# Optimization experiments

Measured on AMD Instinct MI355X. Metric: run time of the kernel, lower is better.

Reference implementation:

```python
import jax, jax.numpy as jnp
import numpy as np

S, E, K, D = 20000, 10000, 128, 128   # students, exercises, knowledge, latent dim
N_EK, N_SE = 40000, 500000            # exercise-knowledge edges, student-exercise edges
B = 2048                              # extract batch size


def setup_inputs() -> dict:
    key = jax.random.key(0)
    ks = jax.random.split(key, 16)
    inp = {}
    # Embedding tables (xavier-ish scale)
    inp["stu_emb"] = jax.random.normal(ks[0], (S, D), jnp.float32) * 0.1
    inp["exer_emb"] = jax.random.normal(ks[1], (E, D), jnp.float32) * 0.1
    inp["kn_emb"] = jax.random.normal(ks[2], (K, D), jnp.float32) * 0.1
    inp["disc_emb"] = jax.random.normal(ks[3], (E, 1), jnp.float32) * 0.1
    # GraphLayer params, stacked over [fusion_layer=2, graph={k_from_e,e_from_k,s_from_e,e_from_s}]
    inp["GW"] = jax.random.normal(ks[4], (2, 4, D, D), jnp.float32) * (1.0 / np.sqrt(D))
    inp["Ga"] = jax.random.normal(ks[5], (2, 4, 2 * D), jnp.float32) * 0.1
    # Fusion attention fcs: idx 0=e_attn_fc1, 1=e_attn_fc2, 2=k_attn_fc3 (weight [2D], bias scalar)
    inp["Fw"] = jax.random.normal(ks[6], (2, 3, 2 * D), jnp.float32) * 0.1
    inp["Fb"] = jax.random.normal(ks[7], (2, 3), jnp.float32) * 0.1
    # q_mask (unused by extract, part of the signature)
    inp["q_mask"] = jax.random.bernoulli(ks[8], 0.03, (B, K)).astype(jnp.float32)
    inp["student_id"] = jax.random.randint(ks[9], (B,), 0, S, jnp.int32)
    inp["exercise_id"] = jax.random.randint(ks[10], (B,), 0, E, jnp.int32)
    # k_from_e graph: nodes = [exercises 0..E) ++ [knowledge E..E+K); edges exercise -> knowledge
    inp["ek_src"] = jax.random.randint(ks[11], (N_EK,), 0, E, jnp.int32)
    inp["ek_dst"] = E + jax.random.randint(ks[12], (N_EK,), 0, K, jnp.int32)
    # s_from_e graph: nodes = [exercises 0..E) ++ [students E..E+S); edges exercise -> student
    inp["se_src"] = jax.random.randint(ks[13], (N_SE,), 0, E, jnp.int32)
    inp["se_dst"] = E + jax.random.randint(ks[14], (N_SE,), 0, S, jnp.int32)
    return inp


def _graph_layer(h, W, a, src, dst, n):
    # GAT-style: z = h W; per-edge score a^T [z_src; z_dst]; segment softmax over dst; weighted sum of z_src.
    z = h @ W                                   # [n, D]
    zs, zd = z[src], z[dst]                     # [ne, D] gathers
    e = jnp.concatenate([zs, zd], axis=1) @ a   # [ne]
    emax = jax.ops.segment_max(e, dst, num_segments=n)
    emax = jnp.where(jnp.isfinite(emax), emax, 0.0)  # empty segments -> -inf -> 0
    ex = jnp.exp(e - emax[dst])
    den = jax.ops.segment_sum(ex, dst, num_segments=n)
    alpha = ex / jnp.where(den > 0, den, 1.0)[dst]
    return jax.ops.segment_sum(alpha[:, None] * zs, dst, num_segments=n)  # nodes w/o mail -> 0 (DGL semantics)


def _fusion(kn, ex, st, GWl, Gal, Fwl, Fbl, ek_src, ek_dst, se_src, se_dst):
    nek, nes = E + K, E + S
    ekg = jnp.concatenate([ex, kn], axis=0)
    kfe = _graph_layer(ekg, GWl[0], Gal[0], ek_src, ek_dst, nek)  # k_from_e
    efk = _graph_layer(ekg, GWl[1], Gal[1], ek_dst, ek_src, nek)  # e_from_k (reversed edges)
    esg = jnp.concatenate([ex, st], axis=0)
    ufe = _graph_layer(esg, GWl[2], Gal[2], se_src, se_dst, nes)  # s_from_e
    efu = _graph_layer(esg, GWl[3], Gal[3], se_dst, se_src, nes)  # e_from_s (reversed edges)
    # knowledge update: softmax over a single column == 1 (faithful to original)
    Dk = kfe[E:]
    s3 = jax.nn.softmax((jnp.concatenate([kn, Dk], axis=1) @ Fwl[2] + Fbl[2])[:, None], axis=1)
    kn2 = kn + s3[:, 0:1] * Dk
    # exercise update: 2-way softmax gate
    Bx, Cx = efk[:E], efu[:E]
    s1 = jnp.concatenate([ex, Bx], axis=1) @ Fwl[0] + Fbl[0]
    s2 = jnp.concatenate([ex, Cx], axis=1) @ Fwl[1] + Fbl[1]
    sc = jax.nn.softmax(jnp.stack([s1, s2], axis=1), axis=1)  # [E, 2]
    ex2 = ex + sc[:, 0:1] * Bx + sc[:, 1:2] * Cx
    st2 = st + ufe[E:]
    return kn2, ex2, st2


def reference(stu_emb, exer_emb, kn_emb, disc_emb, GW, Ga, Fw, Fb, q_mask,
              student_id, exercise_id, ek_src, ek_dst, se_src, se_dst):
    kn, ex, st = kn_emb, exer_emb, stu_emb
    for l in range(2):  # FusionLayer1, FusionLayer2
        kn, ex, st = _fusion(kn, ex, st, GW[l], Ga[l], Fw[l], Fb[l],
                             ek_src, ek_dst, se_src, se_dst)
    bs = st[student_id]            # [B, D]
    be = ex[exercise_id]           # [B, D]
    disc = disc_emb[exercise_id]   # [B, 1]
    # if_type == 'rcd': repeat(1,D).reshape(B,D,D) == broadcast along axis 1
    stu_ts = jnp.broadcast_to(bs[:, None, :], (B, D, D))
    exer_ts = jnp.broadcast_to(be[:, None, :], (B, D, D))
    kn_ts = jnp.broadcast_to(kn[None, :, :], (B, K, D))
    return (stu_ts, exer_ts, disc, kn_ts)
```

## Files before the change

kernel.cpp:

```cpp
#include <hip/hip_runtime.h>

#define S_N 20000
#define E_N 10000
#define K_N 128
#define D_N 128
#define NEK 40000
#define NSE 500000
#define B_N 2048

typedef __attribute__((ext_vector_type(8))) short bf16x8;
typedef __attribute__((ext_vector_type(4))) float f32x4;

__device__ __forceinline__ unsigned short f2bf(float f){
  unsigned int u = __float_as_uint(f);
  unsigned int r = u + 0x7FFFu + ((u >> 16) & 1u);
  return (unsigned short)(r >> 16);
}
__device__ __forceinline__ float bf2f(unsigned short h){
  return __uint_as_float(((unsigned int)h) << 16);
}

struct GS { const unsigned short* Ah; const unsigned short* Al;
            const unsigned short* Wh; const unsigned short* Wl;
            float* Z; int rows; };
struct SSet { const float* z; const float* p; const int* rowptr; const int* col;
              const float* base; float* out; int ndst; };
struct CSet { const int* cnt; int n; int* rp; int* cur; };

__global__ __launch_bounds__(256) void k_wprep(const float* __restrict__ GW, const float* __restrict__ Ga,
                                               unsigned short* __restrict__ wf, float* __restrict__ wa){
  int g = blockIdx.x;
  const float* W  = GW + (size_t)g*16384;
  const float* a1 = Ga + (size_t)g*256;
  unsigned short* whi = wf + (size_t)g*16384;
  unsigned short* wlo = wf + (size_t)(8+g)*16384;
  int t = threadIdx.x, l = t & 63;
  for(int pi = t>>6; pi < 32; pi += 4){
    int c2 = pi >> 2, kt = pi & 3;
    unsigned short h[8], lo[8];
    #pragma unroll
    for(int j=0;j<8;j++){
      int k = kt*32 + (l>>4)*8 + j;
      int c = c2*16 + (l&15);
      float f = W[(size_t)k*128 + c];
      unsigned short hb = f2bf(f);
      h[j] = hb; lo[j] = f2bf(f - bf2f(hb));
    }
    size_t off = ((size_t)pi*64 + l)*8;
    uint4 hv, lv;
    hv.x = (unsigned)h[0] | ((unsigned)h[1]<<16);  hv.y = (unsigned)h[2] | ((unsigned)h[3]<<16);
    hv.z = (unsigned)h[4] | ((unsigned)h[5]<<16);  hv.w = (unsigned)h[6] | ((unsigned)h[7]<<16);
    lv.x = (unsigned)lo[0] | ((unsigned)lo[1]<<16); lv.y = (unsigned)lo[2] | ((unsigned)lo[3]<<16);
    lv.z = (unsigned)lo[4] | ((unsigned)lo[5]<<16); lv.w = (unsigned)lo[6] | ((unsigned)lo[7]<<16);
    *(uint4*)(whi + off) = hv;
    *(uint4*)(wlo + off) = lv;
  }
  for(int k = t; k < 128; k += 256){
    float s = 0.f;
    const float* wr = W + (size_t)k*128;
    for(int c=0;c<128;c++) s += wr[c]*a1[c];
    wa[(size_t)g*128 + k] = s;
  }
}

__global__ __launch_bounds__(256) void k_cvt(const float* __restrict__ kn, const float* __restrict__ ex,
    const float* __restrict__ st,
    unsigned short* __restrict__ knb, unsigned short* __restrict__ exb, unsigned short* __restrict__ stb,
    const float* __restrict__ wa, int l4,
    float* __restrict__ Pefk, float* __restrict__ Pkfe, float* __restrict__ Pufe, float* __restrict__ Pefu){
  int w = (blockIdx.x*256 + threadIdx.x) >> 6;
  int lane = threadIdx.x & 63;
  const float* src; unsigned short *hi, *lo; int r;
  const float* wv1; const float* wv2 = nullptr; float *P1, *P2 = nullptr;
  if(w < K_N){ r = w; src = kn + (size_t)r*128; hi = knb; lo = knb + (size_t)K_N*128;
               wv1 = wa + (size_t)(l4+1)*128; P1 = Pefk; }
  else if(w < K_N + E_N){ r = w - K_N; src = ex + (size_t)r*128; hi = exb; lo = exb + (size_t)E_N*128;
               wv1 = wa + (size_t)(l4+0)*128; P1 = Pkfe;
               wv2 = wa + (size_t)(l4+2)*128; P2 = Pufe; }
  else { r = w - K_N - E_N; if(r >= S_N) return; src = st + (size_t)r*128; hi = stb; lo = stb + (size_t)S_N*128;
               wv1 = wa + (size_t)(l4+3)*128; P1 = Pefu; }
  float2 x = ((const float2*)src)[lane];
  float2 v1 = ((const float2*)wv1)[lane];
  float d1 = x.x*v1.x + x.y*v1.y;
  float d2 = 0.f;
  if(wv2){ float2 v2 = ((const float2*)wv2)[lane]; d2 = x.x*v2.x + x.y*v2.y; }
  #pragma unroll
  for(int off=1; off<64; off<<=1){ d1 += __shfl_xor(d1,off); d2 += __shfl_xor(d2,off); }
  if(lane==0){ P1[r] = expf(d1); if(P2) P2[r] = expf(d2); }
  unsigned short h0 = f2bf(x.x), h1 = f2bf(x.y);
  unsigned short l0 = f2bf(x.x - bf2f(h0)), l1 = f2bf(x.y - bf2f(h1));
  ((ushort2*)(hi + (size_t)r*128))[lane] = make_ushort2(h0,h1);
  ((ushort2*)(lo + (size_t)r*128))[lane] = make_ushort2(l0,l1);
}

#define GT0 4
#define GT1 317
#define GT2 942
#define GT3 1255
__global__ __launch_bounds__(256) void k_gemm(GS g0, GS g1, GS g2, GS g3){
  int b = blockIdx.x;
  GS g; int lt;
  if(b < GT0){ g = g0; lt = b; }
  else if(b < GT1){ g = g1; lt = b - GT0; }
  else if(b < GT2){ g = g2; lt = b - GT1; }
  else { g = g3; lt = b - GT2; }
  int l = threadIdx.x & 63, wv = threadIdx.x >> 6;
  int r0 = lt*32;
  bf16x8 bh[2][4], bl[2][4];
  #pragma unroll
  for(int cs=0; cs<2; cs++)
    #pragma unroll
    for(int kt=0; kt<4; kt++){
      size_t o = (((size_t)((wv*2+cs)*4 + kt))*64 + l)*8;
      bh[cs][kt] = *(const bf16x8*)(g.Wh + o);
      bl[cs][kt] = *(const bf16x8*)(g.Wl + o);
    }
  f32x4 acc[2][2];
  #pragma unroll
  for(int rs=0;rs<2;rs++)
    #pragma unroll
    for(int cs=0;cs<2;cs++) acc[rs][cs] = (f32x4){0.f,0.f,0.f,0.f};
  #pragma unroll
  for(int kt=0; kt<4; kt++){
    bf16x8 ah[2], al[2];
    #pragma unroll
    for(int rs=0; rs<2; rs++){
      size_t ao = ((size_t)(r0 + rs*16 + (l&15)))*128 + kt*32 + (l>>4)*8;
      ah[rs] = *(const bf16x8*)(g.Ah + ao);
      al[rs] = *(const bf16x8*)(g.Al + ao);
    }
    #pragma unroll
    for(int rs=0; rs<2; rs++)
      #pragma unroll
      for(int cs=0; cs<2; cs++){
        acc[rs][cs] = __builtin_amdgcn_mfma_f32_16x16x32_bf16(ah[rs], bh[cs][kt], acc[rs][cs], 0,0,0);
        acc[rs][cs] = __builtin_amdgcn_mfma_f32_16x16x32_bf16(ah[rs], bl[cs][kt], acc[rs][cs], 0,0,0);
        acc[rs][cs] = __builtin_amdgcn_mfma_f32_16x16x32_bf16(al[rs], bh[cs][kt], acc[rs][cs], 0,0,0);
      }
  }
  #pragma unroll
  for(int rs=0; rs<2; rs++)
    #pragma unroll
    for(int cs=0; cs<2; cs++){
      int cb = (wv<<5) + (cs<<4) + (l&15);
      #pragma unroll
      for(int j=0;j<4;j++){
        int rr = r0 + rs*16 + ((l>>4)<<2) + j;
        if(rr < g.rows) g.Z[(size_t)rr*128 + cb] = acc[rs][cs][j];
      }
    }
}

__global__ __launch_bounds__(256) void k_hist(const int* __restrict__ eks, const int* __restrict__ ekd,
      const int* __restrict__ ses, const int* __restrict__ sed,
      int* c_eke, int* c_ekk, int* c_see, int* c_ses){
  int i = blockIdx.x*256 + threadIdx.x;
  if(i < NEK){ atomicAdd(c_eke + eks[i], 1); atomicAdd(c_ekk + (ekd[i]-E_N), 1); }
  if(i < NSE){ atomicAdd(c_see + ses[i], 1); atomicAdd(c_ses + (sed[i]-E_N), 1); }
}

__global__ __launch_bounds__(1024) void k_scan(CSet c0, CSet c1, CSet c2, CSet c3){
  CSet c = c0;
  if(blockIdx.x==1) c=c1; else if(blockIdx.x==2) c=c2; else if(blockIdx.x==3) c=c3;
  __shared__ int part[1024];
  int t = threadIdx.x;
  int n = c.n;
  int chunk = (n + 1023) >> 10;
  int b0 = t * chunk;
  int s = 0;
  for(int i=0;i<chunk;i++){ int idx=b0+i; if(idx<n) s += c.cnt[idx]; }
  part[t] = s;
  __syncthreads();
  for(int off=1; off<1024; off<<=1){
    int v = (t>=off) ? part[t-off] : 0;
    __syncthreads();
    part[t] += v;
    __syncthreads();
  }
  int run = t ? part[t-1] : 0;
  for(int i=0;i<chunk;i++){
    int idx=b0+i;
    if(idx<n){ int cc = c.cnt[idx]; c.rp[idx]=run; c.cur[idx]=run; run += cc; }
  }
  if(t==0) c.rp[n] = part[1023];
}

__global__ __launch_bounds__(256) void k_fill(const int* __restrict__ eks, const int* __restrict__ ekd,
      const int* __restrict__ ses, const int* __restrict__ sed,
      int* u_eke, int* u_ekk, int* u_see, int* u_ses,
      int* o_eke, int* o_ekk, int* o_see, int* o_ses){
  int i = blockIdx.x*256 + threadIdx.x;
  if(i < NEK){
    int a = eks[i], b = ekd[i];
    int pos = atomicAdd(u_eke + a, 1);        o_eke[pos] = b;
    int pos2 = atomicAdd(u_ekk + (b-E_N), 1); o_ekk[pos2] = a;
  }
  if(i < NSE){
    int a = ses[i], b = sed[i];
    int pos = atomicAdd(u_see + a, 1);        o_see[pos] = b;
    int pos2 = atomicAdd(u_ses + (b-E_N), 1); o_ses[pos2] = a;
  }
}

#define SB1 2500
#define SB2 5000
#define SB3 10000
#define SB4 10128
__global__ __launch_bounds__(256) void k_seg(SSet s0, SSet s1, SSet s2, SSet s3){
  __shared__ float4 red[4][32];
  __shared__ float redd[4];
  int b = blockIdx.x;
  int lane = threadIdx.x & 63, wid = threadIdx.x >> 6;
  int half = lane >> 5, l32 = lane & 31;
  SSet s; int row, str, stride; bool multi = false;
  if(b < SB1){ s = s0; row = b*4 + wid; }
  else if(b < SB2){ s = s1; row = (b-SB1)*4 + wid; }
  else if(b < SB3){ s = s2; row = (b-SB2)*4 + wid; }
  else { s = s3; row = b - SB3; multi = true; }
  if(!multi){ str = half; stride = 2; }
  else      { str = wid*2 + half; stride = 8; }
  if(row >= s.ndst) return;
  int e0 = s.rowptr[row], e1 = s.rowptr[row+1];
  const int* col = s.col; const float* p = s.p; const float* z = s.z;
  float4 acc = {0.f,0.f,0.f,0.f}; float den = 0.f;
  int e = e0 + str;
  for(; e + 3*stride < e1; e += 4*stride){
    int cA = col[e], cB = col[e+stride], cC = col[e+2*stride], cD = col[e+3*stride];
    float xA = p[cA], xB = p[cB], xC = p[cC], xD = p[cD];
    float4 zA = ((const float4*)(z + (size_t)cA*128))[l32];
    float4 zB = ((const float4*)(z + (size_t)cB*128))[l32];
    float4 zC = ((const float4*)(z + (size_t)cC*128))[l32];
    float4 zD = ((const float4*)(z + (size_t)cD*128))[l32];
    acc.x += xA*zA.x + xB*zB.x + xC*zC.x + xD*zD.x;
    acc.y += xA*zA.y + xB*zB.y + xC*zC.y + xD*zD.y;
    acc.z += xA*zA.z + xB*zB.z + xC*zC.z + xD*zD.z;
    acc.w += xA*zA.w + xB*zB.w + xC*zC.w + xD*zD.w;
    den += (xA + xB) + (xC + xD);
  }
  for(; e < e1; e += stride){
    int cA = col[e];
    float xA = p[cA];
    float4 zA = ((const float4*)(z + (size_t)cA*128))[l32];
    acc.x += xA*zA.x; acc.y += xA*zA.y; acc.z += xA*zA.z; acc.w += xA*zA.w;
    den += xA;
  }
  acc.x += __shfl_xor(acc.x,32); acc.y += __shfl_xor(acc.y,32);
  acc.z += __shfl_xor(acc.z,32); acc.w += __shfl_xor(acc.w,32);
  den   += __shfl_xor(den,32);
  if(multi){
    if(half==0){ red[wid][l32] = acc; if(l32==0) redd[wid] = den; }
    __syncthreads();
    if(wid) return;
    acc = red[0][l32]; den = redd[0];
    #pragma unroll
    for(int i=1;i<4;i++){
      float4 r4 = red[i][l32];
      acc.x+=r4.x; acc.y+=r4.y; acc.z+=r4.z; acc.w+=r4.w; den += redd[i];
    }
  }
  float inv = den > 0.f ? 1.f/den : 0.f;
  float4 res = {acc.x*inv, acc.y*inv, acc.z*inv, acc.w*inv};
  if(s.base){
    float4 b4 = ((const float4*)(s.base + (size_t)row*128))[l32];
    res.x+=b4.x; res.y+=b4.y; res.z+=b4.z; res.w+=b4.w;
  }
  if(half==0) ((float4*)(s.out + (size_t)row*128))[l32] = res;
}

__global__ __launch_bounds__(256) void k_exup(const float* __restrict__ base, float* __restrict__ ex,
     const float* __restrict__ Bx, const float* __restrict__ Cx,
     const float* __restrict__ Fw, const float* __restrict__ Fb){
  int w = (blockIdx.x*256 + threadIdx.x) >> 6;
  int lane = threadIdx.x & 63;
  if(w >= E_N) return;
  const float* er = base + (size_t)w*128;
  const float* br = Bx + (size_t)w*128;
  const float* cr = Cx + (size_t)w*128;
  float e0 = er[lane], e1 = er[lane+64];
  float b0 = br[lane], b1 = br[lane+64];
  float c0 = cr[lane], c1 = cr[lane+64];
  float s1 = e0*Fw[lane]     + e1*Fw[lane+64]
           + b0*Fw[lane+128] + b1*Fw[lane+192];
  float s2 = e0*Fw[256+lane]     + e1*Fw[256+lane+64]
           + c0*Fw[256+lane+128] + c1*Fw[256+lane+192];
  #pragma unroll
  for(int off=32; off; off>>=1){ s1 += __shfl_down(s1,off); s2 += __shfl_down(s2,off); }
  s1 = __shfl(s1, 0) + Fb[0];
  s2 = __shfl(s2, 0) + Fb[1];
  float mx = fmaxf(s1,s2);
  float pp = expf(s1-mx), qq = expf(s2-mx);
  float inv = 1.f/(pp+qq);
  float* orow = ex + (size_t)w*128;
  orow[lane]    = e0 + (pp*inv)*b0 + (qq*inv)*c0;
  orow[lane+64] = e1 + (pp*inv)*b1 + (qq*inv)*c1;
}

__global__ __launch_bounds__(256) void k_out(const float* __restrict__ st, const float* __restrict__ ex,
    const float* __restrict__ kn, const float* __restrict__ disc,
    const int* __restrict__ sid, const int* __restrict__ eid,
    float* out0, float* out1, float* out2, float* out3){
  int w = (blockIdx.x*256 + threadIdx.x) >> 6;
  int lane = threadIdx.x & 63;
  const int ROWW = 3*B_N*64;
  if(w < ROWW){
    int half = lane>>5, l32 = lane&31;
    int r = w*2 + half;
    int sec = r >> 18;
    int rr = r & 262143;
    int b = rr >> 7, i = rr & 127;
    const float* emb; int srow; float* ob;
    if(sec==0){ emb=st; srow=sid[b]; ob=out0; }
    else if(sec==1){ emb=ex; srow=eid[b]; ob=out1; }
    else { emb=kn; srow=i; ob=out3; }
    f32x4 v = *((const f32x4*)(emb + (size_t)srow*128) + l32);
    __builtin_nontemporal_store(v, (f32x4*)(ob + (size_t)rr*128) + l32);
  } else {
    int i = (w - ROWW)*64 + lane;
    if(i < B_N) out2[i] = disc[eid[i]];
  }
}

extern "C" void kernel_launch(void* const* d_in, const int* in_sizes, int n_in,
                              void* d_out, int out_size, void* d_ws, size_t ws_size,
                              hipStream_t stream){
  (void)in_sizes; (void)out_size; (void)ws_size;
  const float* stu_emb  = (const float*)d_in[0];
  const float* exer_emb = (const float*)d_in[1];
  const float* kn_emb   = (const float*)d_in[2];
  const float* disc_emb = (const float*)d_in[3];
  const float* GW = (const float*)d_in[4];
  const float* Ga = (const float*)d_in[5];
  const float* Fw = (const float*)d_in[6];
  const float* Fb = (const float*)d_in[7];
  int base = n_in - 6;
  const int* sid    = (const int*)d_in[base];
  const int* eid    = (const int*)d_in[base+1];
  const int* ek_src = (const int*)d_in[base+2];
  const int* ek_dst = (const int*)d_in[base+3];
  const int* se_src = (const int*)d_in[base+4];
  const int* se_dst = (const int*)d_in[base+5];

  char* w = (char*)d_ws;
  size_t off = 0;
  auto alloc = [&](size_t bytes)->char*{ char* p = w + off; off += (bytes + 255) & ~(size_t)255; return p; };
  float* st_f = (float*)alloc((size_t)S_N*D_N*4);
  float* ex_f = (float*)alloc((size_t)E_N*D_N*4);
  float* kn_f = (float*)alloc((size_t)K_N*D_N*4);
  float* Bx   = (float*)alloc((size_t)E_N*D_N*4);
  float* Cx   = (float*)alloc((size_t)E_N*D_N*4);
  float* zefk = (float*)alloc((size_t)K_N*D_N*4);
  float* zkfe = (float*)alloc((size_t)E_N*D_N*4);
  float* zefu = (float*)alloc((size_t)S_N*D_N*4);
  float* zufe = (float*)alloc((size_t)E_N*D_N*4);
  float* Pefk = (float*)alloc((size_t)K_N*4);
  float* Pkfe = (float*)alloc((size_t)E_N*4);
  float* Pefu = (float*)alloc((size_t)S_N*4);
  float* Pufe = (float*)alloc((size_t)E_N*4);
  unsigned short* knb = (unsigned short*)alloc((size_t)K_N*D_N*2*2 + 4096);
  unsigned short* exb = (unsigned short*)alloc((size_t)E_N*D_N*2*2 + 4096);
  unsigned short* stb = (unsigned short*)alloc((size_t)S_N*D_N*2*2 + 4096);
  unsigned short* wf  = (unsigned short*)alloc((size_t)16*16384*2);
  float* wa   = (float*)alloc((size_t)8*128*4);
  int*   cnt  = (int*)alloc((size_t)(2*E_N+K_N+S_N)*4);
  int*   rp   = (int*)alloc((size_t)(2*(E_N+1)+(K_N+1)+(S_N+1))*4);
  int*   cur  = (int*)alloc((size_t)(2*E_N+K_N+S_N)*4);
  int*   col  = (int*)alloc((size_t)(2*NEK+2*NSE)*4);

  int* cnt_eke = cnt;                 int* cnt_ekk = cnt + E_N;
  int* cnt_see = cnt + E_N + K_N;     int* cnt_ses = cnt + 2*E_N + K_N;
  int* cur_eke = cur;                 int* cur_ekk = cur + E_N;
  int* cur_see = cur + E_N + K_N;     int* cur_ses = cur + 2*E_N + K_N;
  int* rp_eke = rp;                                int* rp_ekk = rp + (E_N+1);
  int* rp_see = rp + (E_N+1) + (K_N+1);            int* rp_ses = rp + 2*(E_N+1) + (K_N+1);
  int* col_eke = col;                 int* col_ekk = col + NEK;
  int* col_see = col + 2*NEK;         int* col_ses = col + 2*NEK + NSE;

  hipMemsetAsync(cnt, 0, (size_t)(2*E_N+K_N+S_N)*4, stream);
  k_wprep<<<8,256,0,stream>>>(GW, Ga, wf, wa);
  const int gb = (NSE+255)/256;
  k_hist<<<gb,256,0,stream>>>(ek_src, ek_dst, se_src, se_dst, cnt_eke, cnt_ekk, cnt_see, cnt_ses);
  k_scan<<<4,1024,0,stream>>>(CSet{cnt_eke,E_N,rp_eke,cur_eke}, CSet{cnt_ekk,K_N,rp_ekk,cur_ekk},
                              CSet{cnt_see,E_N,rp_see,cur_see}, CSet{cnt_ses,S_N,rp_ses,cur_ses});
  k_fill<<<gb,256,0,stream>>>(ek_src, ek_dst, se_src, se_dst,
                              cur_eke, cur_ekk, cur_see, cur_ses,
                              col_eke, col_ekk, col_see, col_ses);

  const unsigned short* knb_lo = knb + (size_t)K_N*128;
  const unsigned short* exb_lo = exb + (size_t)E_N*128;
  const unsigned short* stb_lo = stb + (size_t)S_N*128;

  for(int l=0; l<2; l++){
    const float* knp = l ? kn_f : kn_emb;
    const float* exp_ = l ? ex_f : exer_emb;
    const float* stp = l ? st_f : stu_emb;
    int l4 = l*4;
    k_cvt<<<(K_N+E_N+S_N)/4,256,0,stream>>>(knp, exp_, stp, knb, exb, stb, wa, l4,
                                            Pefk, Pkfe, Pufe, Pefu);
    GS g0{knb, knb_lo, wf + (size_t)(l4+1)*16384, wf + (size_t)(8+l4+1)*16384, zefk, K_N};
    GS g1{exb, exb_lo, wf + (size_t)(l4+0)*16384, wf + (size_t)(8+l4+0)*16384, zkfe, E_N};
    GS g2{stb, stb_lo, wf + (size_t)(l4+3)*16384, wf + (size_t)(8+l4+3)*16384, zefu, S_N};
    GS g3{exb, exb_lo, wf + (size_t)(l4+2)*16384, wf + (size_t)(8+l4+2)*16384, zufe, E_N};
    k_gemm<<<GT3,256,0,stream>>>(g0,g1,g2,g3);
    SSet s0{zefk - (size_t)E_N*128, Pefk - E_N, rp_eke, col_eke, nullptr, Bx,   E_N};
    SSet s1{zefu - (size_t)E_N*128, Pefu - E_N, rp_see, col_see, nullptr, Cx,   E_N};
    SSet s2{zufe,                   Pufe,       rp_ses, col_ses, stp,     st_f, S_N};
    SSet s3{zkfe,                   Pkfe,       rp_ekk, col_ekk, knp,     kn_f, K_N};
    k_seg<<<SB4,256,0,stream>>>(s0,s1,s2,s3);
    k_exup<<<(E_N*64)/256,256,0,stream>>>(exp_, ex_f, Bx, Cx, Fw + (size_t)l*3*2*D_N, Fb + (size_t)l*3);
  }

  float* out  = (float*)d_out;
  float* out0 = out;
  float* out1 = out0 + (size_t)B_N*D_N*D_N;
  float* out2 = out1 + (size_t)B_N*D_N*D_N;
  float* out3 = out2 + (size_t)B_N;
  int waves = 3*B_N*64 + 32;
  k_out<<<(waves+3)/4,256,0,stream>>>(st_f, ex_f, kn_f, disc_emb, sid, eid, out0, out1, out2, out3);
}
```

Before: 798.5 us.

## Fuse bf16 split conversion and attention scores into GEMM, persistent segment kernel

The separate conversion kernel is removed. The GEMM now reads fp32 activations directly, splits them into hi/lo bf16 in registers, and computes the exp attention score per row alongside the MFMA. Weight prep is folded into the histogram kernel as extra blocks. The segment-softmax kernel moves to a grid-stride layout with fewer blocks. Together these cut kernel launches and the intermediate bf16 buffer traffic, at the cost of redundant conversion work in the GEMM (the exercise rows are converted twice, for g1 and g3) and possibly less parallelism in the segment kernel.

```diff
diff --git a/kernel.cpp b/kernel.cpp
--- a/kernel.cpp
+++ b/kernel.cpp
@@ -19,142 +19,64 @@
 __device__ __forceinline__ float bf2f(unsigned short h){
   return __uint_as_float(((unsigned int)h) << 16);
 }
-
-struct GS { const unsigned short* Ah; const unsigned short* Al;
-            const unsigned short* Wh; const unsigned short* Wl;
-            float* Z; int rows; };
+__device__ __forceinline__ void cvt8(const float* fa, bf16x8& h8, bf16x8& l8){
+  #pragma unroll
+  for(int j=0;j<8;j++){
+    unsigned short hb = f2bf(fa[j]);
+    h8[j] = (short)hb;
+    l8[j] = (short)f2bf(fa[j] - bf2f(hb));
+  }
+}
+
+struct GS { const float* A; const unsigned short* Wh; const unsigned short* Wl;
+            const float* wa; float* Z; float* P; int rows; };
 struct SSet { const float* z; const float* p; const int* rowptr; const int* col;
               const float* base; float* out; int ndst; };
 struct CSet { const int* cnt; int n; int* rp; int* cur; };
 
-__global__ __launch_bounds__(256) void k_wprep(const float* __restrict__ GW, const float* __restrict__ Ga,
-                                               unsigned short* __restrict__ wf, float* __restrict__ wa){
-  int g = blockIdx.x;
-  const float* W  = GW + (size_t)g*16384;
-  const float* a1 = Ga + (size_t)g*256;
-  unsigned short* whi = wf + (size_t)g*16384;
-  unsigned short* wlo = wf + (size_t)(8+g)*16384;
-  int t = threadIdx.x, l = t & 63;
-  for(int pi = t>>6; pi < 32; pi += 4){
-    int c2 = pi >> 2, kt = pi & 3;
-    unsigned short h[8], lo[8];
-    #pragma unroll
-    for(int j=0;j<8;j++){
-      int k = kt*32 + (l>>4)*8 + j;
-      int c = c2*16 + (l&15);
-      float f = W[(size_t)k*128 + c];
-      unsigned short hb = f2bf(f);
-      h[j] = hb; lo[j] = f2bf(f - bf2f(hb));
-    }
-    size_t off = ((size_t)pi*64 + l)*8;
-    uint4 hv, lv;
-    hv.x = (unsigned)h[0] | ((unsigned)h[1]<<16);  hv.y = (unsigned)h[2] | ((unsigned)h[3]<<16);
-    hv.z = (unsigned)h[4] | ((unsigned)h[5]<<16);  hv.w = (unsigned)h[6] | ((unsigned)h[7]<<16);
-    lv.x = (unsigned)lo[0] | ((unsigned)lo[1]<<16); lv.y = (unsigned)lo[2] | ((unsigned)lo[3]<<16);
-    lv.z = (unsigned)lo[4] | ((unsigned)lo[5]<<16); lv.w = (unsigned)lo[6] | ((unsigned)lo[7]<<16);
-    *(uint4*)(whi + off) = hv;
-    *(uint4*)(wlo + off) = lv;
-  }
-  for(int k = t; k < 128; k += 256){
-    float s = 0.f;
-    const float* wr = W + (size_t)k*128;
-    for(int c=0;c<128;c++) s += wr[c]*a1[c];
-    wa[(size_t)g*128 + k] = s;
-  }
-}
-
-__global__ __launch_bounds__(256) void k_cvt(const float* __restrict__ kn, const float* __restrict__ ex,
-    const float* __restrict__ st,
-    unsigned short* __restrict__ knb, unsigned short* __restrict__ exb, unsigned short* __restrict__ stb,
-    const float* __restrict__ wa, int l4,
-    float* __restrict__ Pefk, float* __restrict__ Pkfe, float* __restrict__ Pufe, float* __restrict__ Pefu){
-  int w = (blockIdx.x*256 + threadIdx.x) >> 6;
-  int lane = threadIdx.x & 63;
-  const float* src; unsigned short *hi, *lo; int r;
-  const float* wv1; const float* wv2 = nullptr; float *P1, *P2 = nullptr;
-  if(w < K_N){ r = w; src = kn + (size_t)r*128; hi = knb; lo = knb + (size_t)K_N*128;
-               wv1 = wa + (size_t)(l4+1)*128; P1 = Pefk; }
-  else if(w < K_N + E_N){ r = w - K_N; src = ex + (size_t)r*128; hi = exb; lo = exb + (size_t)E_N*128;
-               wv1 = wa + (size_t)(l4+0)*128; P1 = Pkfe;
-               wv2 = wa + (size_t)(l4+2)*128; P2 = Pufe; }
-  else { r = w - K_N - E_N; if(r >= S_N) return; src = st + (size_t)r*128; hi = stb; lo = stb + (size_t)S_N*128;
-               wv1 = wa + (size_t)(l4+3)*128; P1 = Pefu; }
-  float2 x = ((const float2*)src)[lane];
-  float2 v1 = ((const float2*)wv1)[lane];
-  float d1 = x.x*v1.x + x.y*v1.y;
-  float d2 = 0.f;
-  if(wv2){ float2 v2 = ((const float2*)wv2)[lane]; d2 = x.x*v2.x + x.y*v2.y; }
-  #pragma unroll
-  for(int off=1; off<64; off<<=1){ d1 += __shfl_xor(d1,off); d2 += __shfl_xor(d2,off); }
-  if(lane==0){ P1[r] = expf(d1); if(P2) P2[r] = expf(d2); }
-  unsigned short h0 = f2bf(x.x), h1 = f2bf(x.y);
-  unsigned short l0 = f2bf(x.x - bf2f(h0)), l1 = f2bf(x.y - bf2f(h1));
-  ((ushort2*)(hi + (size_t)r*128))[lane] = make_ushort2(h0,h1);
-  ((ushort2*)(lo + (size_t)r*128))[lane] = make_ushort2(l0,l1);
-}
-
-#define GT0 4
-#define GT1 317
-#define GT2 942
-#define GT3 1255
-__global__ __launch_bounds__(256) void k_gemm(GS g0, GS g1, GS g2, GS g3){
-  int b = blockIdx.x;
-  GS g; int lt;
-  if(b < GT0){ g = g0; lt = b; }
-  else if(b < GT1){ g = g1; lt = b - GT0; }
-  else if(b < GT2){ g = g2; lt = b - GT1; }
-  else { g = g3; lt = b - GT2; }
-  int l = threadIdx.x & 63, wv = threadIdx.x >> 6;
-  int r0 = lt*32;
-  bf16x8 bh[2][4], bl[2][4];
-  #pragma unroll
-  for(int cs=0; cs<2; cs++)
-    #pragma unroll
-    for(int kt=0; kt<4; kt++){
-      size_t o = (((size_t)((wv*2+cs)*4 + kt))*64 + l)*8;
-      bh[cs][kt] = *(const bf16x8*)(g.Wh + o);
-      bl[cs][kt] = *(const bf16x8*)(g.Wl + o);
-    }
-  f32x4 acc[2][2];
-  #pragma unroll
-  for(int rs=0;rs<2;rs++)
-    #pragma unroll
-    for(int cs=0;cs<2;cs++) acc[rs][cs] = (f32x4){0.f,0.f,0.f,0.f};
-  #pragma unroll
-  for(int kt=0; kt<4; kt++){
-    bf16x8 ah[2], al[2];
-    #pragma unroll
-    for(int rs=0; rs<2; rs++){
-      size_t ao = ((size_t)(r0 + rs*16 + (l&15)))*128 + kt*32 + (l>>4)*8;
-      ah[rs] = *(const bf16x8*)(g.Ah + ao);
-      al[rs] = *(const bf16x8*)(g.Al + ao);
-    }
-    #pragma unroll
-    for(int rs=0; rs<2; rs++)
-      #pragma unroll
-      for(int cs=0; cs<2; cs++){
-        acc[rs][cs] = __builtin_amdgcn_mfma_f32_16x16x32_bf16(ah[rs], bh[cs][kt], acc[rs][cs], 0,0,0);
-        acc[rs][cs] = __builtin_amdgcn_mfma_f32_16x16x32_bf16(ah[rs], bl[cs][kt], acc[rs][cs], 0,0,0);
-        acc[rs][cs] = __builtin_amdgcn_mfma_f32_16x16x32_bf16(al[rs], bh[cs][kt], acc[rs][cs], 0,0,0);
-      }
-  }
-  #pragma unroll
-  for(int rs=0; rs<2; rs++)
-    #pragma unroll
-    for(int cs=0; cs<2; cs++){
-      int cb = (wv<<5) + (cs<<4) + (l&15);
-      #pragma unroll
-      for(int j=0;j<4;j++){
-        int rr = r0 + rs*16 + ((l>>4)<<2) + j;
-        if(rr < g.rows) g.Z[(size_t)rr*128 + cb] = acc[rs][cs][j];
-      }
-    }
-}
-
+#define HB ((NSE+255)/256)
 __global__ __launch_bounds__(256) void k_hist(const int* __restrict__ eks, const int* __restrict__ ekd,
       const int* __restrict__ ses, const int* __restrict__ sed,
-      int* c_eke, int* c_ekk, int* c_see, int* c_ses){
-  int i = blockIdx.x*256 + threadIdx.x;
+      int* c_eke, int* c_ekk, int* c_see, int* c_ses,
+      const float* __restrict__ GW, const float* __restrict__ Ga,
+      unsigned short* __restrict__ wf, float* __restrict__ wa){
+  int bb = blockIdx.x;
+  if(bb >= HB){
+    int g = bb - HB;
+    const float* W  = GW + (size_t)g*16384;
+    const float* a1 = Ga + (size_t)g*256;
+    unsigned short* whi = wf + (size_t)g*16384;
+    unsigned short* wlo = wf + (size_t)(8+g)*16384;
+    int t = threadIdx.x, l = t & 63;
+    for(int pi = t>>6; pi < 32; pi += 4){
+      int c2 = pi >> 2, kt = pi & 3;
+      unsigned short h[8], lo[8];
+      #pragma unroll
+      for(int j=0;j<8;j++){
+        int k = kt*32 + (l>>4)*8 + j;
+        int c = c2*16 + (l&15);
+        float f = W[(size_t)k*128 + c];
+        unsigned short hb = f2bf(f);
+        h[j] = hb; lo[j] = f2bf(f - bf2f(hb));
+      }
+      size_t off = ((size_t)pi*64 + l)*8;
+      uint4 hv, lv;
+      hv.x = (unsigned)h[0] | ((unsigned)h[1]<<16);  hv.y = (unsigned)h[2] | ((unsigned)h[3]<<16);
+      hv.z = (unsigned)h[4] | ((unsigned)h[5]<<16);  hv.w = (unsigned)h[6] | ((unsigned)h[7]<<16);
+      lv.x = (unsigned)lo[0] | ((unsigned)lo[1]<<16); lv.y = (unsigned)lo[2] | ((unsigned)lo[3]<<16);
+      lv.z = (unsigned)lo[4] | ((unsigned)lo[5]<<16); lv.w = (unsigned)lo[6] | ((unsigned)lo[7]<<16);
+      *(uint4*)(whi + off) = hv;
+      *(uint4*)(wlo + off) = lv;
+    }
+    for(int k = t; k < 128; k += 256){
+      float s = 0.f;
+      const float* wr = W + (size_t)k*128;
+      for(int c=0;c<128;c++) s += wr[c]*a1[c];
+      wa[(size_t)g*128 + k] = s;
+    }
+    return;
+  }
+  int i = bb*256 + threadIdx.x;
   if(i < NEK){ atomicAdd(c_eke + eks[i], 1); atomicAdd(c_ekk + (ekd[i]-E_N), 1); }
   if(i < NSE){ atomicAdd(c_see + ses[i], 1); atomicAdd(c_ses + (sed[i]-E_N), 1); }
 }
@@ -202,52 +124,132 @@
   }
 }
 
-#define SB1 2500
-#define SB2 5000
-#define SB3 10000
-#define SB4 10128
+#define GT0 4
+#define GT1 317
+#define GT2 942
+#define GT3 1255
+__global__ __launch_bounds__(256) void k_gemm(GS g0, GS g1, GS g2, GS g3){
+  int b = blockIdx.x;
+  GS g; int lt;
+  if(b < GT0){ g = g0; lt = b; }
+  else if(b < GT1){ g = g1; lt = b - GT0; }
+  else if(b < GT2){ g = g2; lt = b - GT1; }
+  else { g = g3; lt = b - GT2; }
+  int l = threadIdx.x & 63, wv = threadIdx.x >> 6;
+  int r0 = lt*32;
+  bf16x8 bh[2][4], bl[2][4];
+  #pragma unroll
+  for(int cs=0; cs<2; cs++)
+    #pragma unroll
+    for(int kt=0; kt<4; kt++){
+      size_t o = (((size_t)((wv*2+cs)*4 + kt))*64 + l)*8;
+      bh[cs][kt] = *(const bf16x8*)(g.Wh + o);
+      bl[cs][kt] = *(const bf16x8*)(g.Wl + o);
+    }
+  f32x4 acc[2][2];
+  #pragma unroll
+  for(int rs=0;rs<2;rs++)
+    #pragma unroll
+    for(int cs=0;cs<2;cs++) acc[rs][cs] = (f32x4){0.f,0.f,0.f,0.f};
+  float pacc[2] = {0.f, 0.f};
+  #pragma unroll
+  for(int kt=0; kt<4; kt++){
+    bf16x8 ah[2], al[2];
+    #pragma unroll
+    for(int rs=0; rs<2; rs++){
+      int row = r0 + rs*16 + (l&15);
+      float fa[8];
+      if(row < g.rows){
+        const float* ap = g.A + (size_t)row*128 + kt*32 + ((l>>4)<<3);
+        float4 f0 = *(const float4*)ap;
+        float4 f1 = *(const float4*)(ap+4);
+        fa[0]=f0.x; fa[1]=f0.y; fa[2]=f0.z; fa[3]=f0.w;
+        fa[4]=f1.x; fa[5]=f1.y; fa[6]=f1.z; fa[7]=f1.w;
+      } else {
+        #pragma unroll
+        for(int j=0;j<8;j++) fa[j]=0.f;
+      }
+      const float* wap = g.wa + kt*32 + ((l>>4)<<3);
+      float4 w0 = *(const float4*)wap;
+      float4 w1 = *(const float4*)(wap+4);
+      pacc[rs] += fa[0]*w0.x + fa[1]*w0.y + fa[2]*w0.z + fa[3]*w0.w
+                + fa[4]*w1.x + fa[5]*w1.y + fa[6]*w1.z + fa[7]*w1.w;
+      cvt8(fa, ah[rs], al[rs]);
+    }
+    #pragma unroll
+    for(int rs=0; rs<2; rs++)
+      #pragma unroll
+      for(int cs=0; cs<2; cs++){
+        acc[rs][cs] = __builtin_amdgcn_mfma_f32_16x16x32_bf16(ah[rs], bh[cs][kt], acc[rs][cs], 0,0,0);
+        acc[rs][cs] = __builtin_amdgcn_mfma_f32_16x16x32_bf16(ah[rs], bl[cs][kt], acc[rs][cs], 0,0,0);
+        acc[rs][cs] = __builtin_amdgcn_mfma_f32_16x16x32_bf16(al[rs], bh[cs][kt], acc[rs][cs], 0,0,0);
+      }
+  }
+  #pragma unroll
+  for(int rs=0; rs<2; rs++)
+    #pragma unroll
+    for(int cs=0; cs<2; cs++){
+      int cb = (wv<<5) + (cs<<4) + (l&15);
+      #pragma unroll
+      for(int j=0;j<4;j++){
+        int rr = r0 + rs*16 + ((l>>4)<<2) + j;
+        if(rr < g.rows) g.Z[(size_t)rr*128 + cb] = acc[rs][cs][j];
+      }
+    }
+  #pragma unroll
+  for(int rs=0; rs<2; rs++){
+    float s = pacc[rs];
+    s += __shfl_xor(s,16); s += __shfl_xor(s,32);
+    int r = r0 + rs*16 + (l&15);
+    if(l < 16 && r < g.rows) g.P[r] = expf(s);
+  }
+}
+
+#define SGB0 256
+#define SGB1 568
+#define SGB2 1193
+#define SGB3 1321
 __global__ __launch_bounds__(256) void k_seg(SSet s0, SSet s1, SSet s2, SSet s3){
   __shared__ float4 red[4][32];
   __shared__ float redd[4];
   int b = blockIdx.x;
   int lane = threadIdx.x & 63, wid = threadIdx.x >> 6;
   int half = lane >> 5, l32 = lane & 31;
-  SSet s; int row, str, stride; bool multi = false;
-  if(b < SB1){ s = s0; row = b*4 + wid; }
-  else if(b < SB2){ s = s1; row = (b-SB1)*4 + wid; }
-  else if(b < SB3){ s = s2; row = (b-SB2)*4 + wid; }
-  else { s = s3; row = b - SB3; multi = true; }
-  if(!multi){ str = half; stride = 2; }
-  else      { str = wid*2 + half; stride = 8; }
-  if(row >= s.ndst) return;
-  int e0 = s.rowptr[row], e1 = s.rowptr[row+1];
+  SSet s; int wg = 0, nw = 0; bool multi = false;
+  if(b < SGB0){ s = s0; wg = b*4 + wid; nw = SGB0*4; }
+  else if(b < SGB1){ s = s1; wg = (b-SGB0)*4 + wid; nw = (SGB1-SGB0)*4; }
+  else if(b < SGB2){ s = s2; wg = (b-SGB1)*4 + wid; nw = (SGB2-SGB1)*4; }
+  else { s = s3; multi = true; }
   const int* col = s.col; const float* p = s.p; const float* z = s.z;
-  float4 acc = {0.f,0.f,0.f,0.f}; float den = 0.f;
-  int e = e0 + str;
-  for(; e + 3*stride < e1; e += 4*stride){
-    int cA = col[e], cB = col[e+stride], cC = col[e+2*stride], cD = col[e+3*stride];
-    float xA = p[cA], xB = p[cB], xC = p[cC], xD = p[cD];
-    float4 zA = ((const float4*)(z + (size_t)cA*128))[l32];
-    float4 zB = ((const float4*)(z + (size_t)cB*128))[l32];
-    float4 zC = ((const float4*)(z + (size_t)cC*128))[l32];
-    float4 zD = ((const float4*)(z + (size_t)cD*128))[l32];
-    acc.x += xA*zA.x + xB*zB.x + xC*zC.x + xD*zD.x;
-    acc.y += xA*zA.y + xB*zB.y + xC*zC.y + xD*zD.y;
-    acc.z += xA*zA.z + xB*zB.z + xC*zC.z + xD*zD.z;
-    acc.w += xA*zA.w + xB*zB.w + xC*zC.w + xD*zD.w;
-    den += (xA + xB) + (xC + xD);
-  }
-  for(; e < e1; e += stride){
-    int cA = col[e];
-    float xA = p[cA];
-    float4 zA = ((const float4*)(z + (size_t)cA*128))[l32];
-    acc.x += xA*zA.x; acc.y += xA*zA.y; acc.z += xA*zA.z; acc.w += xA*zA.w;
-    den += xA;
-  }
-  acc.x += __shfl_xor(acc.x,32); acc.y += __shfl_xor(acc.y,32);
-  acc.z += __shfl_xor(acc.z,32); acc.w += __shfl_xor(acc.w,32);
-  den   += __shfl_xor(den,32);
   if(multi){
+    int row = b - SGB2;
+    int e0 = s.rowptr[row], e1 = s.rowptr[row+1];
+    float4 acc = {0.f,0.f,0.f,0.f}; float den = 0.f;
+    int str = wid*2 + half;
+    int e = e0 + str;
+    for(; e + 24 < e1; e += 32){
+      int cA = col[e], cB = col[e+8], cC = col[e+16], cD = col[e+24];
+      float xA = p[cA], xB = p[cB], xC = p[cC], xD = p[cD];
+      float4 zA = ((const float4*)(z + (size_t)cA*128))[l32];
+      float4 zB = ((const float4*)(z + (size_t)cB*128))[l32];
+      float4 zC = ((const float4*)(z + (size_t)cC*128))[l32];
+      float4 zD = ((const float4*)(z + (size_t)cD*128))[l32];
+      acc.x += xA*zA.x + xB*zB.x + xC*zC.x + xD*zD.x;
+      acc.y += xA*zA.y + xB*zB.y + xC*zC.y + xD*zD.y;
+      acc.z += xA*zA.z + xB*zB.z + xC*zC.z + xD*zD.z;
+      acc.w += xA*zA.w + xB*zB.w + xC*zC.w + xD*zD.w;
+      den += (xA + xB) + (xC + xD);
+    }
+    for(; e < e1; e += 8){
+      int cA = col[e];
+      float xA = p[cA];
+      float4 zA = ((const float4*)(z + (size_t)cA*128))[l32];
+      acc.x += xA*zA.x; acc.y += xA*zA.y; acc.z += xA*zA.z; acc.w += xA*zA.w;
+      den += xA;
+    }
+    acc.x += __shfl_xor(acc.x,32); acc.y += __shfl_xor(acc.y,32);
+    acc.z += __shfl_xor(acc.z,32); acc.w += __shfl_xor(acc.w,32);
+    den   += __shfl_xor(den,32);
     if(half==0){ red[wid][l32] = acc; if(l32==0) redd[wid] = den; }
     __syncthreads();
     if(wid) return;
@@ -257,14 +259,50 @@
       float4 r4 = red[i][l32];
       acc.x+=r4.x; acc.y+=r4.y; acc.z+=r4.z; acc.w+=r4.w; den += redd[i];
     }
-  }
-  float inv = den > 0.f ? 1.f/den : 0.f;
-  float4 res = {acc.x*inv, acc.y*inv, acc.z*inv, acc.w*inv};
-  if(s.base){
-    float4 b4 = ((const float4*)(s.base + (size_t)row*128))[l32];
-    res.x+=b4.x; res.y+=b4.y; res.z+=b4.z; res.w+=b4.w;
-  }
-  if(half==0) ((float4*)(s.out + (size_t)row*128))[l32] = res;
+    float inv = den > 0.f ? 1.f/den : 0.f;
+    float4 res = {acc.x*inv, acc.y*inv, acc.z*inv, acc.w*inv};
+    if(s.base){
+      float4 b4 = ((const float4*)(s.base + (size_t)row*128))[l32];
+      res.x+=b4.x; res.y+=b4.y; res.z+=b4.z; res.w+=b4.w;
+    }
+    if(half==0) ((float4*)(s.out + (size_t)row*128))[l32] = res;
+    return;
+  }
+  for(int row = wg; row < s.ndst; row += nw){
+    int e0 = s.rowptr[row], e1 = s.rowptr[row+1];
+    float4 acc = {0.f,0.f,0.f,0.f}; float den = 0.f;
+    int e = e0 + half;
+    for(; e + 6 < e1; e += 8){
+      int cA = col[e], cB = col[e+2], cC = col[e+4], cD = col[e+6];
+      float xA = p[cA], xB = p[cB], xC = p[cC], xD = p[cD];
+      float4 zA = ((const float4*)(z + (size_t)cA*128))[l32];
+      float4 zB = ((const float4*)(z + (size_t)cB*128))[l32];
+      float4 zC = ((const float4*)(z + (size_t)cC*128))[l32];
+      float4 zD = ((const float4*)(z + (size_t)cD*128))[l32];
+      acc.x += xA*zA.x + xB*zB.x + xC*zC.x + xD*zD.x;
+      acc.y += xA*zA.y + xB*zB.y + xC*zC.y + xD*zD.y;
+      acc.z += xA*zA.z + xB*zB.z + xC*zC.z + xD*zD.z;
+      acc.w += xA*zA.w + xB*zB.w + xC*zC.w + xD*zD.w;
+      den += (xA + xB) + (xC + xD);
+    }
+    for(; e < e1; e += 2){
+      int cA = col[e];
+      float xA = p[cA];
+      float4 zA = ((const float4*)(z + (size_t)cA*128))[l32];
+      acc.x += xA*zA.x; acc.y += xA*zA.y; acc.z += xA*zA.z; acc.w += xA*zA.w;
+      den += xA;
+    }
+    acc.x += __shfl_xor(acc.x,32); acc.y += __shfl_xor(acc.y,32);
+    acc.z += __shfl_xor(acc.z,32); acc.w += __shfl_xor(acc.w,32);
+    den   += __shfl_xor(den,32);
+    float inv = den > 0.f ? 1.f/den : 0.f;
+    float4 res = {acc.x*inv, acc.y*inv, acc.z*inv, acc.w*inv};
+    if(s.base){
+      float4 b4 = ((const float4*)(s.base + (size_t)row*128))[l32];
+      res.x+=b4.x; res.y+=b4.y; res.z+=b4.z; res.w+=b4.w;
+    }
+    if(half==0) ((float4*)(s.out + (size_t)row*128))[l32] = res;
+  }
 }
 
 __global__ __launch_bounds__(256) void k_exup(const float* __restrict__ base, float* __restrict__ ex,
@@ -356,10 +394,7 @@
   float* Pkfe = (float*)alloc((size_t)E_N*4);
   float* Pefu = (float*)alloc((size_t)S_N*4);
   float* Pufe = (float*)alloc((size_t)E_N*4);
-  unsigned short* knb = (unsigned short*)alloc((size_t)K_N*D_N*2*2 + 4096);
-  unsigned short* exb = (unsigned short*)alloc((size_t)E_N*D_N*2*2 + 4096);
-  unsigned short* stb = (unsigned short*)alloc((size_t)S_N*D_N*2*2 + 4096);
-  unsigned short* wf  = (unsigned short*)alloc((size_t)16*16384*2);
+  unsigned short* wf = (unsigned short*)alloc((size_t)16*16384*2);
   float* wa   = (float*)alloc((size_t)8*128*4);
   int*   cnt  = (int*)alloc((size_t)(2*E_N+K_N+S_N)*4);
   int*   rp   = (int*)alloc((size_t)(2*(E_N+1)+(K_N+1)+(S_N+1))*4);
@@ -376,36 +411,30 @@
   int* col_see = col + 2*NEK;         int* col_ses = col + 2*NEK + NSE;
 
   hipMemsetAsync(cnt, 0, (size_t)(2*E_N+K_N+S_N)*4, stream);
-  k_wprep<<<8,256,0,stream>>>(GW, Ga, wf, wa);
-  const int gb = (NSE+255)/256;
-  k_hist<<<gb,256,0,stream>>>(ek_src, ek_dst, se_src, se_dst, cnt_eke, cnt_ekk, cnt_see, cnt_ses);
+  k_hist<<<HB+8,256,0,stream>>>(ek_src, ek_dst, se_src, se_dst,
+                                cnt_eke, cnt_ekk, cnt_see, cnt_ses,
+                                GW, Ga, wf, wa);
   k_scan<<<4,1024,0,stream>>>(CSet{cnt_eke,E_N,rp_eke,cur_eke}, CSet{cnt_ekk,K_N,rp_ekk,cur_ekk},
                               CSet{cnt_see,E_N,rp_see,cur_see}, CSet{cnt_ses,S_N,rp_ses,cur_ses});
-  k_fill<<<gb,256,0,stream>>>(ek_src, ek_dst, se_src, se_dst,
+  k_fill<<<HB,256,0,stream>>>(ek_src, ek_dst, se_src, se_dst,
                               cur_eke, cur_ekk, cur_see, cur_ses,
                               col_eke, col_ekk, col_see, col_ses);
-
-  const unsigned short* knb_lo = knb + (size_t)K_N*128;
-  const unsigned short* exb_lo = exb + (size_t)E_N*128;
-  const unsigned short* stb_lo = stb + (size_t)S_N*128;
 
   for(int l=0; l<2; l++){
     const float* knp = l ? kn_f : kn_emb;
     const float* exp_ = l ? ex_f : exer_emb;
     const float* stp = l ? st_f : stu_emb;
     int l4 = l*4;
-    k_cvt<<<(K_N+E_N+S_N)/4,256,0,stream>>>(knp, exp_, stp, knb, exb, stb, wa, l4,
-                                            Pefk, Pkfe, Pufe, Pefu);
-    GS g0{knb, knb_lo, wf + (size_t)(l4+1)*16384, wf + (size_t)(8+l4+1)*16384, zefk, K_N};
-    GS g1{exb, exb_lo, wf + (size_t)(l4+0)*16384, wf + (size_t)(8+l4+0)*16384, zkfe, E_N};
-    GS g2{stb, stb_lo, wf + (size_t)(l4+3)*16384, wf + (size_t)(8+l4+3)*16384, zefu, S_N};
-    GS g3{exb, exb_lo, wf + (size_t)(l4+2)*16384, wf + (size_t)(8+l4+2)*16384, zufe, E_N};
+    GS g0{knp,  wf + (size_t)(l4+1)*16384, wf + (size_t)(8+l4+1)*16384, wa + (size_t)(l4+1)*128, zefk, Pefk, K_N};
+    GS g1{exp_, wf + (size_t)(l4+0)*16384, wf + (size_t)(8+l4+0)*16384, wa + (size_t)(l4+0)*128, zkfe, Pkfe, E_N};
+    GS g2{stp,  wf + (size_t)(l4+3)*16384, wf + (size_t)(8+l4+3)*16384, wa + (size_t)(l4+3)*128, zefu, Pefu, S_N};
+    GS g3{exp_, wf + (size_t)(l4+2)*16384, wf + (size_t)(8+l4+2)*16384, wa + (size_t)(l4+2)*128, zufe, Pufe, E_N};
     k_gemm<<<GT3,256,0,stream>>>(g0,g1,g2,g3);
     SSet s0{zefk - (size_t)E_N*128, Pefk - E_N, rp_eke, col_eke, nullptr, Bx,   E_N};
     SSet s1{zefu - (size_t)E_N*128, Pefu - E_N, rp_see, col_see, nullptr, Cx,   E_N};
     SSet s2{zufe,                   Pufe,       rp_ses, col_ses, stp,     st_f, S_N};
     SSet s3{zkfe,                   Pkfe,       rp_ekk, col_ekk, knp,     kn_f, K_N};
-    k_seg<<<SB4,256,0,stream>>>(s0,s1,s2,s3);
+    k_seg<<<SGB3,256,0,stream>>>(s0,s1,s2,s3);
     k_exup<<<(E_N*64)/256,256,0,stream>>>(exp_, ex_f, Bx, Cx, Fw + (size_t)l*3*2*D_N, Fb + (size_t)l*3);
   }
 
```

After: 821.9 us. +2.9%, slower.
